# Kernel tuning notes

Hardware: AMD Instinct MI355X
Metric: run time of the kernel (lower is better)

Reference implementation:

```python
import jax, jax.numpy as jnp
import numpy as np

D_MODEL = 1024
HEADS = 16
D_FF = 4096
EPS = 1e-6
NEG = -1e9


def setup_inputs() -> dict:
    key = jax.random.key(0)
    ks = jax.random.split(key, 12)
    B, S, D = 2, 2048, D_MODEL
    s = 0.02
    return {
        "x": jax.random.normal(ks[0], (B, S, D), dtype=jnp.float32),
        "mask": jax.random.randint(ks[1], (B, 1, S), 0, 2, dtype=jnp.int32),
        "alpha1": jnp.ones((D,), jnp.float32),
        "bias1": jnp.zeros((D,), jnp.float32),
        "alpha2": jnp.ones((D,), jnp.float32),
        "bias2": jnp.zeros((D,), jnp.float32),
        "Wk": jax.random.normal(ks[2], (D, D), jnp.float32) * s,
        "bk": jnp.zeros((D,), jnp.float32),
        "Wv": jax.random.normal(ks[3], (D, D), jnp.float32) * s,
        "bv": jnp.zeros((D,), jnp.float32),
        "Wo": jax.random.normal(ks[4], (D, D), jnp.float32) * s,
        "bo": jnp.zeros((D,), jnp.float32),
        "W1": jax.random.normal(ks[5], (D, D_FF), jnp.float32) * s,
        "b1": jnp.zeros((D_FF,), jnp.float32),
        "W2": jax.random.normal(ks[6], (D_FF, D), jnp.float32) * s,
        "b2": jnp.zeros((D,), jnp.float32),
    }


def _norm(x, alpha, bias):
    # torch Norm: unbiased std (ddof=1), eps added to std (not variance)
    mu = jnp.mean(x, axis=-1, keepdims=True)
    sd = jnp.std(x, axis=-1, keepdims=True, ddof=1)
    return alpha * (x - mu) / (sd + EPS) + bias


def reference(x, mask, alpha1, bias1, alpha2, bias2,
              Wk, bk, Wv, bv, Wo, bo, W1, b1, W2, b2):
    B, S, D = x.shape
    H, dk = HEADS, D // HEADS

    x2 = _norm(x, alpha1, bias1)
    # NOTE: source bug preserved: q uses k_linear weights
    q = (x2 @ Wk + bk).reshape(B, S, H, dk).transpose(0, 2, 1, 3)  # [B,H,S,dk]
    k = (x2 @ Wk + bk).reshape(B, S, H, dk).transpose(0, 2, 1, 3)
    v = (x2 @ Wv + bv).reshape(B, S, H, dk).transpose(0, 2, 1, 3)

    scores = jnp.einsum('bhqd,bhkd->bhqk', q, k) / jnp.sqrt(jnp.float32(dk))
    scores = jnp.where(mask[:, None, :, :] == 0, NEG, scores)  # [B,1,1,S] broadcast
    attn = jax.nn.softmax(scores, axis=-1)
    ctx = jnp.einsum('bhqk,bhkd->bhqd', attn, v)
    concat = ctx.transpose(0, 2, 1, 3).reshape(B, S, D)
    x = x + (concat @ Wo + bo)

    x2 = _norm(x, alpha2, bias2)
    ff = jax.nn.relu(x2 @ W1 + b1) @ W2 + b2
    return x + ff
```

## Files before the change

### kernel.cpp

```cpp
#include <hip/hip_runtime.h>
#include <hip/hip_bf16.h>
#include <math.h>

typedef __bf16 bf16_t;
typedef __bf16 bf16x8 __attribute__((ext_vector_type(8)));
typedef __bf16 bf16x4 __attribute__((ext_vector_type(4)));
typedef float  f32x4  __attribute__((ext_vector_type(4)));

#define MFMA16(a,b,c) __builtin_amdgcn_mfma_f32_16x16x32_bf16((a),(b),(c),0,0,0)

__device__ static inline void gload_lds16(const void* g, void* l) {
    __builtin_amdgcn_global_load_lds((const __attribute__((address_space(1))) void*)g,
                                     (__attribute__((address_space(3))) void*)l, 16, 0, 0);
}

__device__ static inline float exp2_hw(float x) {
#if __has_builtin(__builtin_amdgcn_exp2f)
    return __builtin_amdgcn_exp2f(x);
#else
    float r; asm("v_exp_f32 %0, %1" : "=v"(r) : "v"(x)); return r;
#endif
}

__global__ __launch_bounds__(256)
void preamble_k(const float* __restrict__ Wk, const float* __restrict__ Wv,
                const float* __restrict__ Wo, const float* __restrict__ W1,
                const float* __restrict__ W2,
                bf16_t* __restrict__ WkT, bf16_t* __restrict__ WvT,
                bf16_t* __restrict__ WoT, bf16_t* __restrict__ W1T,
                bf16_t* __restrict__ W2T,
                const float* __restrict__ bk, const float* __restrict__ bv,
                float* __restrict__ bkv,
                const int* __restrict__ msk, float* __restrict__ mbias)
{
    __shared__ float t[32][33];
    const int id = blockIdx.x;
    if (id < 11264) {
        const float* in; bf16_t* out; int R, C, bx, by;
        if (id < 3072) {
            R = 1024; C = 1024;
            const int wsel = id >> 10, lid = id & 1023;
            in  = (wsel == 0) ? Wk : (wsel == 1) ? Wv : Wo;
            out = (wsel == 0) ? WkT : (wsel == 1) ? WvT : WoT;
            bx = lid & 31; by = lid >> 5;
        } else if (id < 7168) {
            R = 1024; C = 4096; const int lid = id - 3072;
            in = W1; out = W1T;
            bx = lid & 127; by = lid >> 7;
        } else {
            R = 4096; C = 1024; const int lid = id - 7168;
            in = W2; out = W2T;
            bx = lid & 31; by = lid >> 5;
        }
        const int tx = threadIdx.x & 31, ty = threadIdx.x >> 5;
        const int r0 = by << 5, c0 = bx << 5;
#pragma unroll
        for (int i = 0; i < 4; ++i)
            t[ty + i*8][tx] = in[(size_t)(r0 + ty + i*8) * C + c0 + tx];
        __syncthreads();
#pragma unroll
        for (int i = 0; i < 4; ++i)
            out[(size_t)(c0 + ty + i*8) * R + r0 + tx] = (bf16_t)t[tx][ty + i*8];
    } else if (id < 11272) {
        const int i = (id - 11264) * 256 + threadIdx.x;
        bkv[i] = (i < 1024) ? bk[i] : bv[i - 1024];
    } else {
        const int i = (id - 11272) * 256 + threadIdx.x;
        mbias[i] = (msk[i] == 0) ? -16384.0f : -16.0f;
    }
}

__global__ __launch_bounds__(256)
void layernorm_k(const float* __restrict__ x, const float* __restrict__ gam,
                 const float* __restrict__ bet, bf16_t* __restrict__ out)
{
    const int row = blockIdx.x, tid = threadIdx.x;
    const float4 v = ((const float4*)(x + (size_t)row * 1024))[tid];
    float s  = v.x + v.y + v.z + v.w;
    float ss = v.x*v.x + v.y*v.y + v.z*v.z + v.w*v.w;
#pragma unroll
    for (int off = 32; off >= 1; off >>= 1) {
        s  += __shfl_xor(s,  off);
        ss += __shfl_xor(ss, off);
    }
    __shared__ float rs[4], rq[4];
    if ((tid & 63) == 0) { rs[tid >> 6] = s; rq[tid >> 6] = ss; }
    __syncthreads();
    s  = rs[0] + rs[1] + rs[2] + rs[3];
    ss = rq[0] + rq[1] + rq[2] + rq[3];
    const float mu  = s * (1.0f / 1024.0f);
    const float var = fmaxf((ss - 1024.0f * mu * mu) * (1.0f / 1023.0f), 0.0f);
    const float inv = 1.0f / (sqrtf(var) + 1e-6f);
    const int c = tid << 2;
    bf16x4 o;
    o[0] = (bf16_t)(gam[c+0] * ((v.x - mu) * inv) + bet[c+0]);
    o[1] = (bf16_t)(gam[c+1] * ((v.y - mu) * inv) + bet[c+1]);
    o[2] = (bf16_t)(gam[c+2] * ((v.z - mu) * inv) + bet[c+2]);
    o[3] = (bf16_t)(gam[c+3] * ((v.w - mu) * inv) + bet[c+3]);
    *(bf16x4*)(out + (size_t)row * 1024 + c) = o;
}

template<bool RELU, bool RES, int NFR, bool DBUF, bool VT>
__global__ __launch_bounds__(256, 2)
void gemm128(const bf16_t* __restrict__ A, const bf16_t* __restrict__ Bt,
             const float* __restrict__ bias, const float* __restrict__ res,
             bf16_t* __restrict__ Cb, float* __restrict__ Cf,
             bf16_t* __restrict__ Cv,
             int M, int N, int K)
{
    constexpr int NTILE = NFR * 32;
    constexpr int NBUF = DBUF ? 2 : 1;
    __shared__ __align__(16) bf16_t As[NBUF][128 * 64];
    __shared__ __align__(16) bf16_t Bs[NBUF][NTILE * 64];
    const int tid  = threadIdx.x;
    const int lane = tid & 63;
    const int wid  = tid >> 6;
    const int wr = wid >> 1, wc = wid & 1;
    const int ntn = N / NTILE;
    const int cpx = gridDim.x >> 3;
    const int swz = (blockIdx.x & 7) * cpx + (blockIdx.x >> 3);
    const int bm = (swz / ntn) << 7;
    const int bn = (swz % ntn) * NTILE;
    const int l15 = lane & 15;
    const int g   = lane >> 4;

    f32x4 acc[4][NFR];
#pragma unroll
    for (int i = 0; i < 4; ++i)
#pragma unroll
        for (int j = 0; j < NFR; ++j)
#pragma unroll
            for (int e = 0; e < 4; ++e) acc[i][j][e] = 0.0f;

    const int srow = tid >> 3;
    const int scb  = (((tid & 7) << 4) ^ ((srow & 7) << 4));
    const bf16_t* Ab = A  + (size_t)(bm + srow) * K + (scb >> 1);
    const bf16_t* Bb = Bt + (size_t)(bn + srow) * K + (scb >> 1);

    auto stage = [&](int buf, int kt) {
        const int k0 = kt << 6;
        bf16_t* AsB = As[buf] + wid * 512;
        bf16_t* BsB = Bs[buf] + wid * 512;
#pragma unroll
        for (int it = 0; it < 4; ++it)
            gload_lds16(Ab + k0 + (size_t)(it * 32) * K, AsB + it * 2048);
#pragma unroll
        for (int it = 0; it < NFR; ++it)
            gload_lds16(Bb + k0 + (size_t)(it * 32) * K, BsB + it * 2048);
    };

    auto compute = [&](int buf) {
        bf16x8 af[4][2], bfr[NFR][2];
#pragma unroll
        for (int mi = 0; mi < 4; ++mi) {
            const int ar = (wr << 6) + mi * 16 + l15;
#pragma unroll
            for (int ks = 0; ks < 2; ++ks) {
                const int kb = (ks << 6) + (g << 4);
                af[mi][ks] = *(const bf16x8*)((const char*)As[buf] + ar * 128 + (kb ^ ((ar & 7) << 4)));
            }
        }
#pragma unroll
        for (int ni = 0; ni < NFR; ++ni) {
            const int br = wc * (NFR * 16) + ni * 16 + l15;
#pragma unroll
            for (int ks = 0; ks < 2; ++ks) {
                const int kb = (ks << 6) + (g << 4);
                bfr[ni][ks] = *(const bf16x8*)((const char*)Bs[buf] + br * 128 + (kb ^ ((br & 7) << 4)));
            }
        }
#pragma unroll
        for (int mi = 0; mi < 4; ++mi)
#pragma unroll
            for (int ni = 0; ni < NFR; ++ni) {
                acc[mi][ni] = MFMA16(af[mi][0], bfr[ni][0], acc[mi][ni]);
                acc[mi][ni] = MFMA16(af[mi][1], bfr[ni][1], acc[mi][ni]);
            }
    };

    const int nK = K >> 6;
    if constexpr (DBUF) {
        stage(0, 0);
        __syncthreads();
        for (int kt = 0; kt < nK; ++kt) {
            const int cur = kt & 1;
            if (kt + 1 < nK) stage(cur ^ 1, kt + 1);
            compute(cur);
            __syncthreads();
        }
    } else {
        for (int kt = 0; kt < nK; ++kt) {
            stage(0, kt);
            __syncthreads();
            compute(0);
            __syncthreads();
        }
    }

    if (VT && bn >= 1024) {
#pragma unroll
        for (int mi = 0; mi < 4; ++mi)
#pragma unroll
            for (int ni = 0; ni < NFR; ++ni) {
                const int gc = bn - 1024 + wc * (NFR * 16) + ni * 16 + l15;
                const float bv = bias[gc + 1024];
                bf16x4 o;
#pragma unroll
                for (int j = 0; j < 4; ++j) o[j] = (bf16_t)(acc[mi][ni][j] + bv);
                *(bf16x4*)(Cv + (size_t)gc * 4096 + bm + (wr << 6) + mi * 16 + (g << 2)) = o;
            }
        return;
    }

#pragma unroll
    for (int mi = 0; mi < 4; ++mi)
#pragma unroll
        for (int ni = 0; ni < NFR; ++ni) {
            const int gc = bn + wc * (NFR * 16) + ni * 16 + l15;
            const float bv = bias[gc];
#pragma unroll
            for (int j = 0; j < 4; ++j) {
                const int gr = bm + (wr << 6) + mi * 16 + (g << 2) + j;
                float vv = acc[mi][ni][j] + bv;
                if (RELU) vv = fmaxf(vv, 0.0f);
                if (RES)  Cf[(size_t)gr * N + gc] = vv + res[(size_t)gr * N + gc];
                else      Cb[(size_t)gr * N + gc] = (bf16_t)vv;
            }
        }
}

__global__ __launch_bounds__(256, 4)
void gemm64(const bf16_t* __restrict__ A, const bf16_t* __restrict__ Bt,
            const float* __restrict__ bias, const float* __restrict__ res,
            float* __restrict__ Cf, int M, int N, int K)
{
    __shared__ __align__(16) bf16_t As[2][64 * 64];
    __shared__ __align__(16) bf16_t Bs[2][64 * 64];
    const int tid  = threadIdx.x;
    const int lane = tid & 63;
    const int wid  = tid >> 6;
    const int wr = wid >> 1, wc = wid & 1;
    const int ntn = N >> 6;
    const int cpx = gridDim.x >> 3;
    const int swz = (blockIdx.x & 7) * cpx + (blockIdx.x >> 3);
    const int bm = (swz / ntn) << 6;
    const int bn = (swz % ntn) << 6;
    const int l15 = lane & 15;
    const int g   = lane >> 4;

    f32x4 acc[2][2];
#pragma unroll
    for (int i = 0; i < 2; ++i)
#pragma unroll
        for (int j = 0; j < 2; ++j)
#pragma unroll
            for (int e = 0; e < 4; ++e) acc[i][j][e] = 0.0f;

    const int srow = tid >> 3;
    const int scb  = (((tid & 7) << 4) ^ ((srow & 7) << 4));
    const bf16_t* Ab = A  + (size_t)(bm + srow) * K + (scb >> 1);
    const bf16_t* Bb = Bt + (size_t)(bn + srow) * K + (scb >> 1);

    auto stage = [&](int buf, int kt) {
        const int k0 = kt << 6;
        bf16_t* AsB = As[buf] + wid * 512;
        bf16_t* BsB = Bs[buf] + wid * 512;
#pragma unroll
        for (int it = 0; it < 2; ++it)
            gload_lds16(Ab + k0 + (size_t)(it * 32) * K, AsB + it * 2048);
#pragma unroll
        for (int it = 0; it < 2; ++it)
            gload_lds16(Bb + k0 + (size_t)(it * 32) * K, BsB + it * 2048);
    };

    auto compute = [&](int buf) {
        bf16x8 af[2][2], bfr[2][2];
#pragma unroll
        for (int mi = 0; mi < 2; ++mi) {
            const int ar = (wr << 5) + mi * 16 + l15;
#pragma unroll
            for (int ks = 0; ks < 2; ++ks) {
                const int kb = (ks << 6) + (g << 4);
                af[mi][ks] = *(const bf16x8*)((const char*)As[buf] + ar * 128 + (kb ^ ((ar & 7) << 4)));
            }
        }
#pragma unroll
        for (int ni = 0; ni < 2; ++ni) {
            const int br = (wc << 5) + ni * 16 + l15;
#pragma unroll
            for (int ks = 0; ks < 2; ++ks) {
                const int kb = (ks << 6) + (g << 4);
                bfr[ni][ks] = *(const bf16x8*)((const char*)Bs[buf] + br * 128 + (kb ^ ((br & 7) << 4)));
            }
        }
#pragma unroll
        for (int mi = 0; mi < 2; ++mi)
#pragma unroll
            for (int ni = 0; ni < 2; ++ni) {
                acc[mi][ni] = MFMA16(af[mi][0], bfr[ni][0], acc[mi][ni]);
                acc[mi][ni] = MFMA16(af[mi][1], bfr[ni][1], acc[mi][ni]);
            }
    };

    const int nK = K >> 6;
    stage(0, 0);
    __syncthreads();
    for (int kt = 0; kt < nK; ++kt) {
        const int cur = kt & 1;
        if (kt + 1 < nK) stage(cur ^ 1, kt + 1);
        compute(cur);
        __syncthreads();
    }

#pragma unroll
    for (int mi = 0; mi < 2; ++mi)
#pragma unroll
        for (int ni = 0; ni < 2; ++ni) {
            const int gc = bn + (wc << 5) + ni * 16 + l15;
            const float bv = bias[gc];
#pragma unroll
            for (int j = 0; j < 4; ++j) {
                const int gr = bm + (wr << 5) + mi * 16 + (g << 2) + j;
                Cf[(size_t)gr * N + gc] = acc[mi][ni][j] + bv + res[(size_t)gr * N + gc];
            }
        }
}

__global__ __launch_bounds__(256, 3)
void attn_kernel(const bf16_t* __restrict__ qkv, const bf16_t* __restrict__ vT,
                 const float* __restrict__ mbias, bf16_t* __restrict__ ctx)
{
    __shared__ __align__(16) bf16_t Ks[2][64 * 64];
    __shared__ __align__(16) bf16_t Vs[2][64 * 64];
    __shared__ __align__(16) char   Ps[4][4096];

    const int tid = threadIdx.x, lane = tid & 63, wid = tid >> 6;
    const int l15 = lane & 15, g = lane >> 4;
    const int id = blockIdx.x;
    const int qt = (id >> 3) & 15;
    const int bh = (id & 7) * 4 + (id >> 7);
    const int b = bh >> 4, h = bh & 15;
    const size_t rowQ = (size_t)(b * 2048 + qt * 128 + wid * 32);
    const float C = 0.18033688f;

    bf16x8 qf[2][2];
#pragma unroll
    for (int qfi = 0; qfi < 2; ++qfi)
#pragma unroll
        for (int ks = 0; ks < 2; ++ks)
            qf[qfi][ks] = *(const bf16x8*)(qkv + (rowQ + qfi*16 + l15) * 2048
                                           + h*64 + ks*32 + g*8);

    bf16x8 vones;
#pragma unroll
    for (int e = 0; e < 8; ++e) vones[e] = (bf16_t)1.0f;

    f32x4 O[2][4], l_acc[2];
#pragma unroll
    for (int mf = 0; mf < 2; ++mf) {
#pragma unroll
        for (int df = 0; df < 4; ++df)
#pragma unroll
            for (int e = 0; e < 4; ++e) O[mf][df][e] = 0.0f;
#pragma unroll
        for (int e = 0; e < 4; ++e) l_acc[mf][e] = 0.0f;
    }

    const int srow = tid >> 3;
    const int scb  = (((tid & 7) << 4) ^ ((srow & 7) << 4));
    const bf16_t* Kb = qkv + (size_t)(b*2048 + srow) * 2048 + h*64 + (scb >> 1);
    const bf16_t* Vb = vT  + (size_t)(h*64 + srow) * 4096 + b*2048 + (scb >> 1);
    const float*  Mb = mbias + b*2048;
    bf16_t* Ks0 = Ks[0] + wid * 512;  bf16_t* Ks1 = Ks[1] + wid * 512;
    bf16_t* Vs0 = Vs[0] + wid * 512;  bf16_t* Vs1 = Vs[1] + wid * 512;

    #define STAGE(KD, VD, KT)                                        \
        do {                                                         \
            gload_lds16(Kb + (size_t)(KT) * 2048, (KD));             \
            gload_lds16(Kb + (size_t)((KT) + 32) * 2048, (KD) + 2048);\
            gload_lds16(Vb + (KT), (VD));                            \
            gload_lds16(Vb + (size_t)32 * 4096 + (KT), (VD) + 2048); \
        } while (0)

    STAGE(Ks0, Vs0, 0);
    __syncthreads();

    char* Pw = Ps[wid];

    for (int kt_i = 0; kt_i < 32; ++kt_i) {
        const int kt = kt_i << 6;
        const bool cur1 = (kt_i & 1);
        if (kt_i < 31) {
            if (cur1) STAGE(Ks0, Vs0, kt + 64);
            else      STAGE(Ks1, Vs1, kt + 64);
        }
        const char* Kc = (const char*)(cur1 ? Ks[1] : Ks[0]);
        const char* Vc = (const char*)(cur1 ? Vs[1] : Vs[0]);

        bf16x8 kf[4][2];
#pragma unroll
        for (int kfi = 0; kfi < 4; ++kfi) {
            const int kr = kfi*16 + l15;
#pragma unroll
            for (int ks = 0; ks < 2; ++ks)
                kf[kfi][ks] = *(const bf16x8*)(Kc + kr*128
                                               + ((ks*64 + g*16) ^ ((kr & 7) << 4)));
        }
        f32x4 st[4][2];
#pragma unroll
        for (int kfi = 0; kfi < 4; ++kfi)
#pragma unroll
            for (int qfi = 0; qfi < 2; ++qfi) {
                f32x4 t;
#pragma unroll
                for (int e = 0; e < 4; ++e) t[e] = 0.0f;
                t = MFMA16(kf[kfi][0], qf[qfi][0], t);
                t = MFMA16(kf[kfi][1], qf[qfi][1], t);
                st[kfi][qfi] = t;
            }

        bf16x8 vf[4][2];
#pragma unroll
        for (int df = 0; df < 4; ++df) {
            const int vr = df*16 + l15;
#pragma unroll
            for (int ks = 0; ks < 2; ++ks)
                vf[df][ks] = *(const bf16x8*)(Vc + vr*128
                                              + ((ks*64 + g*16) ^ ((vr & 7) << 4)));
        }

#pragma unroll
        for (int kfi = 0; kfi < 4; ++kfi) {
            const float4 bb = *(const float4*)(Mb + kt + kfi*16 + g*4);
            const float* bj = (const float*)&bb;
#pragma unroll
            for (int qfi = 0; qfi < 2; ++qfi) {
                const int q = qfi*16 + l15;
                bf16x4 pk;
#pragma unroll
                for (int j = 0; j < 4; ++j)
                    pk[j] = (bf16_t)exp2_hw(fmaf(st[kfi][qfi][j], C, bj[j]));
                *(bf16x4*)(Pw + q*128 + ((kfi*32 + g*8) ^ ((l15 & 7) << 4))) = pk;
            }
        }
        bf16x8 pa[2][2];
#pragma unroll
        for (int mf = 0; mf < 2; ++mf) {
            const int r = mf*16 + l15;
#pragma unroll
            for (int ks = 0; ks < 2; ++ks)
                pa[mf][ks] = *(const bf16x8*)(Pw + r*128 + ((ks*64 + g*16) ^ ((l15 & 7) << 4)));
        }
#pragma unroll
        for (int mf = 0; mf < 2; ++mf) {
#pragma unroll
            for (int df = 0; df < 4; ++df) {
                O[mf][df] = MFMA16(pa[mf][0], vf[df][0], O[mf][df]);
                O[mf][df] = MFMA16(pa[mf][1], vf[df][1], O[mf][df]);
            }
            l_acc[mf] = MFMA16(pa[mf][0], vones, l_acc[mf]);
            l_acc[mf] = MFMA16(pa[mf][1], vones, l_acc[mf]);
        }
        __syncthreads();
    }
    #undef STAGE

#pragma unroll
    for (int mf = 0; mf < 2; ++mf)
#pragma unroll
        for (int j = 0; j < 4; ++j) {
            const float ri = __builtin_amdgcn_rcpf(l_acc[mf][j]);
            const size_t gr = rowQ + mf*16 + g*4 + j;
#pragma unroll
            for (int df = 0; df < 4; ++df)
                ctx[gr * 1024 + h*64 + df*16 + l15] = (bf16_t)(O[mf][df][j] * ri);
        }
}

extern "C" void kernel_launch(void* const* d_in, const int* in_sizes, int n_in,
                              void* d_out, int out_size, void* d_ws, size_t ws_size,
                              hipStream_t stream)
{
    const float* x   = (const float*)d_in[0];
    const int*   msk = (const int*)  d_in[1];
    const float* a1  = (const float*)d_in[2];
    const float* be1 = (const float*)d_in[3];
    const float* a2  = (const float*)d_in[4];
    const float* be2 = (const float*)d_in[5];
    const float* Wk  = (const float*)d_in[6];
    const float* bk  = (const float*)d_in[7];
    const float* Wv  = (const float*)d_in[8];
    const float* bv  = (const float*)d_in[9];
    const float* Wo  = (const float*)d_in[10];
    const float* bo  = (const float*)d_in[11];
    const float* W1  = (const float*)d_in[12];
    const float* b1  = (const float*)d_in[13];
    const float* W2  = (const float*)d_in[14];
    const float* b2  = (const float*)d_in[15];
    float* out = (float*)d_out;

    char* ws = (char*)d_ws;
    const size_t MB = 1u << 20;
    if (ws_size < 78 * MB) return;
    bf16_t* WkT = (bf16_t*)(ws + 0 * MB);
    bf16_t* WvT = (bf16_t*)(ws + 2 * MB);
    bf16_t* WoT = (bf16_t*)(ws + 4 * MB);
    bf16_t* W1T = (bf16_t*)(ws + 6 * MB);
    bf16_t* W2T = (bf16_t*)(ws + 14 * MB);
    bf16_t* x2  = (bf16_t*)(ws + 22 * MB);
    bf16_t* qkv = (bf16_t*)(ws + 30 * MB);
    bf16_t* vTb = (bf16_t*)(ws + 46 * MB);
    bf16_t* ctx = (bf16_t*)(ws + 54 * MB);
    float*  xn  = (float*) (ws + 62 * MB);
    float*  bkv   = (float*)(ws + 62 * MB);
    float*  mbias = (float*)(ws + 62 * MB + 32768);
    bf16_t* hb  = (bf16_t*)(ws + 30 * MB);

    dim3 blk(256);
    preamble_k<<<dim3(11288), blk, 0, stream>>>(Wk, Wv, Wo, W1, W2,
                                                WkT, WvT, WoT, W1T, W2T,
                                                bk, bv, bkv, msk, mbias);

    layernorm_k<<<4096, blk, 0, stream>>>(x, a1, be1, x2);
    gemm128<false,false,4,true,true><<<dim3(32 * 16), blk, 0, stream>>>(x2, WkT, bkv, nullptr, qkv, nullptr, vTb, 4096, 2048, 1024);
    attn_kernel<<<dim3(512), blk, 0, stream>>>(qkv, vTb, mbias, ctx);
    gemm64<<<dim3(64 * 16), blk, 0, stream>>>(ctx, WoT, bo, x, xn, 4096, 1024, 1024);
    layernorm_k<<<4096, blk, 0, stream>>>(xn, a2, be2, x2);
    gemm128<true,false,4,false,false><<<dim3(32 * 32), blk, 0, stream>>>(x2, W1T, b1, nullptr, hb, nullptr, nullptr, 4096, 4096, 1024);
    gemm64<<<dim3(64 * 16), blk, 0, stream>>>(hb, W2T, b2, xn, out, 4096, 1024, 4096);
}
```

Measured before the change: 217.1 us.

## Split attention key range across two blocks and add a combine kernel

The attention kernel now launches twice as many blocks, and each one processes half of the key sequence. Each block writes an unnormalized bf16 partial output and its row sums to workspace. A new combine kernel adds the two halves and divides by the summed denominator. The goal is better occupancy and CU fill, since 512 blocks under-fill the device. The cost is an extra kernel launch, extra global traffic for the partials, and the precision loss of storing unnormalized partials in bf16. Workspace buffers are reassigned so the partials reuse regions that are dead at that point.

```diff
diff --git a/kernel.cpp b/kernel.cpp
--- a/kernel.cpp
+++ b/kernel.cpp
@@ -328,7 +328,8 @@
 
 __global__ __launch_bounds__(256, 3)
 void attn_kernel(const bf16_t* __restrict__ qkv, const bf16_t* __restrict__ vT,
-                 const float* __restrict__ mbias, bf16_t* __restrict__ ctx)
+                 const float* __restrict__ mbias, bf16_t* __restrict__ Op,
+                 float* __restrict__ lp)
 {
     __shared__ __align__(16) bf16_t Ks[2][64 * 64];
     __shared__ __align__(16) bf16_t Vs[2][64 * 64];
@@ -337,8 +338,9 @@
     const int tid = threadIdx.x, lane = tid & 63, wid = tid >> 6;
     const int l15 = lane & 15, g = lane >> 4;
     const int id = blockIdx.x;
-    const int qt = (id >> 3) & 15;
-    const int bh = (id & 7) * 4 + (id >> 7);
+    const int qt   = (id >> 3) & 15;
+    const int half = (id >> 7) & 1;
+    const int bh   = (id & 7) * 4 + (id >> 8);
     const int b = bh >> 4, h = bh & 15;
     const size_t rowQ = (size_t)(b * 2048 + qt * 128 + wid * 32);
     const float C = 0.18033688f;
@@ -382,15 +384,16 @@
             gload_lds16(Vb + (size_t)32 * 4096 + (KT), (VD) + 2048); \
         } while (0)
 
-    STAGE(Ks0, Vs0, 0);
+    const int kt0 = half << 10;
+    STAGE(Ks0, Vs0, kt0);
     __syncthreads();
 
     char* Pw = Ps[wid];
 
-    for (int kt_i = 0; kt_i < 32; ++kt_i) {
-        const int kt = kt_i << 6;
+    for (int kt_i = 0; kt_i < 16; ++kt_i) {
+        const int kt = kt0 + (kt_i << 6);
         const bool cur1 = (kt_i & 1);
-        if (kt_i < 31) {
+        if (kt_i < 15) {
             if (cur1) STAGE(Ks0, Vs0, kt + 64);
             else      STAGE(Ks1, Vs1, kt + 64);
         }
@@ -465,16 +468,40 @@
     }
     #undef STAGE
 
+    bf16_t* Ob = Op + (size_t)half * (4096u * 1024u);
 #pragma unroll
     for (int mf = 0; mf < 2; ++mf)
 #pragma unroll
         for (int j = 0; j < 4; ++j) {
-            const float ri = __builtin_amdgcn_rcpf(l_acc[mf][j]);
             const size_t gr = rowQ + mf*16 + g*4 + j;
 #pragma unroll
             for (int df = 0; df < 4; ++df)
-                ctx[gr * 1024 + h*64 + df*16 + l15] = (bf16_t)(O[mf][df][j] * ri);
-        }
+                Ob[gr * 1024 + h*64 + df*16 + l15] = (bf16_t)O[mf][df][j];
+            if (l15 == 0)
+                lp[half*65536 + (b*16 + h)*2048 + (qt*128 + wid*32) + mf*16 + g*4 + j]
+                    = l_acc[mf][j];
+        }
+}
+
+__global__ __launch_bounds__(256)
+void attn_combine(const bf16_t* __restrict__ Op, const float* __restrict__ lp,
+                  bf16_t* __restrict__ ctx)
+{
+    const int row = blockIdx.x;
+    const int t = threadIdx.x;
+    const int b = row >> 11, q = row & 2047;
+    const int h = t >> 4, d0 = (t & 15) << 2;
+    const int li = (b*16 + h)*2048 + q;
+    const float l = lp[li] + lp[65536 + li];
+    const float ri = __builtin_amdgcn_rcpf(l);
+    const size_t off = (size_t)row * 1024 + h*64 + d0;
+    const bf16x4 o1 = *(const bf16x4*)(Op + off);
+    const bf16x4 o2 = *(const bf16x4*)(Op + (size_t)4096*1024 + off);
+    bf16x4 o;
+#pragma unroll
+    for (int j = 0; j < 4; ++j)
+        o[j] = (bf16_t)(((float)o1[j] + (float)o2[j]) * ri);
+    *(bf16x4*)(ctx + off) = o;
 }
 
 extern "C" void kernel_launch(void* const* d_in, const int* in_sizes, int n_in,
@@ -508,12 +535,14 @@
     bf16_t* W1T = (bf16_t*)(ws + 6 * MB);
     bf16_t* W2T = (bf16_t*)(ws + 14 * MB);
     bf16_t* x2  = (bf16_t*)(ws + 22 * MB);
+    float*  lp  = (float*) (ws + 22 * MB);
     bf16_t* qkv = (bf16_t*)(ws + 30 * MB);
     bf16_t* vTb = (bf16_t*)(ws + 46 * MB);
     bf16_t* ctx = (bf16_t*)(ws + 54 * MB);
+    float*  bkv   = (float*)(ws + 54 * MB);
+    float*  mbias = (float*)(ws + 54 * MB + 32768);
     float*  xn  = (float*) (ws + 62 * MB);
-    float*  bkv   = (float*)(ws + 62 * MB);
-    float*  mbias = (float*)(ws + 62 * MB + 32768);
+    bf16_t* Op  = (bf16_t*)(ws + 62 * MB);
     bf16_t* hb  = (bf16_t*)(ws + 30 * MB);
 
     dim3 blk(256);
@@ -523,7 +552,8 @@
 
     layernorm_k<<<4096, blk, 0, stream>>>(x, a1, be1, x2);
     gemm128<false,false,4,true,true><<<dim3(32 * 16), blk, 0, stream>>>(x2, WkT, bkv, nullptr, qkv, nullptr, vTb, 4096, 2048, 1024);
-    attn_kernel<<<dim3(512), blk, 0, stream>>>(qkv, vTb, mbias, ctx);
+    attn_kernel<<<dim3(1024), blk, 0, stream>>>(qkv, vTb, mbias, Op, lp);
+    attn_combine<<<dim3(4096), blk, 0, stream>>>(Op, lp, ctx);
     gemm64<<<dim3(64 * 16), blk, 0, stream>>>(ctx, WoT, bo, x, xn, 4096, 1024, 1024);
     layernorm_k<<<4096, blk, 0, stream>>>(xn, a2, be2, x2);
     gemm128<true,false,4,false,false><<<dim3(32 * 32), blk, 0, stream>>>(x2, W1T, b1, nullptr, hb, nullptr, nullptr, 4096, 4096, 1024);
```

New measurement: 223.5 us. 3.0% more time.
